# Optimization experiments

Measured on AMD Instinct MI355X. Metric: run time of the kernel, lower is better.

## Reference

```python
import jax, jax.numpy as jnp
import numpy as np
from jax import lax

B, S, H, T = 64, 512, 1024, 48


def setup_inputs() -> dict:
    key = jax.random.key(0)
    ks = jax.random.split(key, 8)
    x = jax.random.normal(ks[0], (B, S, H), dtype=jnp.float32)
    # left-aligned variable-length attention mask (lengths in [S//2, S])
    lengths = jax.random.randint(ks[1], (B,), S // 2, S + 1)
    attention_mask = (jnp.arange(S)[None, :] < lengths[:, None]).astype(jnp.int32)
    labels = jax.random.randint(ks[2], (B, S), 0, T).astype(jnp.int64)
    # decoder Linear(H, T)
    W = jax.random.normal(ks[3], (H, T), dtype=jnp.float32) / np.sqrt(H)
    b = jnp.zeros((T,), dtype=jnp.float32)
    # CRF parameters (allennlp-style: transitions + start/end transitions)
    transitions = jax.random.normal(ks[4], (T, T), dtype=jnp.float32) * 0.1
    start_trans = jax.random.normal(ks[5], (T,), dtype=jnp.float32) * 0.1
    end_trans = jax.random.normal(ks[6], (T,), dtype=jnp.float32) * 0.1
    return {"x": x, "attention_mask": attention_mask, "labels": labels,
            "W": W, "b": b, "transitions": transitions,
            "start_trans": start_trans, "end_trans": end_trans}


def _log_partition(logits, mask, trans, start, end):
    # logits [B,S,T], mask [B,S] int. Returns logZ [B].
    alpha0 = start[None, :] + logits[:, 0]                     # [B,T]
    emits = jnp.moveaxis(logits[:, 1:], 1, 0)                  # [S-1,B,T]
    ms = mask[:, 1:].T                                         # [S-1,B]

    def step(alpha, inp):
        emit, m = inp
        inner = alpha[:, :, None] + trans[None, :, :] + emit[:, None, :]  # [B,T,T]
        new = jax.nn.logsumexp(inner, axis=1)
        alpha = jnp.where(m[:, None] > 0, new, alpha)
        return alpha, None

    alpha, _ = lax.scan(step, alpha0, (emits, ms))
    return jax.nn.logsumexp(alpha + end[None, :], axis=1)      # [B]


def _gold_score(logits, labels, mask, trans, start, end):
    maskf = mask.astype(logits.dtype)
    emit = jnp.take_along_axis(logits, labels[..., None], axis=2)[..., 0]  # [B,S]
    emit_score = jnp.sum(emit * maskf, axis=1)
    tr = trans[labels[:, :-1], labels[:, 1:]]                   # [B,S-1]
    trans_score = jnp.sum(tr * maskf[:, 1:], axis=1)
    last_idx = jnp.sum(mask, axis=1) - 1                        # [B]
    last_tags = jnp.take_along_axis(labels, last_idx[:, None], axis=1)[:, 0]
    return start[labels[:, 0]] + emit_score + trans_score + end[last_tags]


def _viterbi(logits, mask, trans, start, end):
    Bn, Sn, Tn = logits.shape
    v0 = start[None, :] + logits[:, 0]
    emits = jnp.moveaxis(logits[:, 1:], 1, 0)                  # [S-1,B,T]
    ms = mask[:, 1:].T
    ident = jnp.broadcast_to(jnp.arange(Tn, dtype=jnp.int32)[None, :], (Bn, Tn))

    def step(v, inp):
        emit, m = inp
        scores = v[:, :, None] + trans[None, :, :]              # [B,T_prev,T_cur]
        bp = jnp.argmax(scores, axis=1).astype(jnp.int32)       # [B,T]
        best = jnp.max(scores, axis=1) + emit
        v_new = jnp.where(m[:, None] > 0, best, v)
        bp = jnp.where(m[:, None] > 0, bp, ident)               # identity at padded steps
        return v_new, bp

    v, bps = lax.scan(step, v0, (emits, ms))                    # bps [S-1,B,T]
    last = jnp.argmax(v + end[None, :], axis=1).astype(jnp.int32)  # [B]

    def back(tag, bp):
        prev = jnp.take_along_axis(bp, tag[:, None], axis=1)[:, 0]
        return prev, tag

    first_tag, rest = lax.scan(back, last, bps, reverse=True)   # rest [S-1,B]
    tags = jnp.concatenate([first_tag[:, None], rest.T], axis=1)  # [B,S]
    return (tags * mask).astype(jnp.int64)                      # pad with zeros


def reference(x, attention_mask, labels, W, b, transitions, start_trans, end_trans):
    features = jnp.einsum('bsh,ht->bst', x, W) + b              # decoder Linear
    pred_labels = _viterbi(features, attention_mask, transitions, start_trans, end_trans)
    logZ = _log_partition(features, attention_mask, transitions, start_trans, end_trans)
    gold = _gold_score(features, labels, attention_mask, transitions, start_trans, end_trans)
    loss = -jnp.sum(gold - logZ)                                # -log-likelihood, summed over batch
    return features, pred_labels, loss
```

## Files before the change

### kernel.cpp

```cpp
#include <hip/hip_runtime.h>
#include <hip/hip_bf16.h>
#include <math.h>

#define Bn 64
#define Sn 512
#define Hn 1024
#define Tn 48

#define LOG2E 1.4426950408889634f
#define LN2f  0.6931471805599453f

#define PRED_OFF (Bn*Sn*Tn)
#define LOSS_OFF (PRED_OFF + Bn*Sn)

#define RL(x,i) __int_as_float(__builtin_amdgcn_readlane(__float_as_int(x),(i)))

#if __has_builtin(__builtin_amdgcn_exp2f)
#define EXP2(x) __builtin_amdgcn_exp2f(x)
#else
#define EXP2(x) exp2f(x)
#endif
#if __has_builtin(__builtin_amdgcn_logf)
#define LOG2(x) __builtin_amdgcn_logf(x)
#else
#define LOG2(x) log2f(x)
#endif

#define DOT4(ACC,A,B) { ACC = fmaf((A).x,(B).x,ACC); ACC = fmaf((A).y,(B).y,ACC); ACC = fmaf((A).z,(B).z,ACC); ACC = fmaf((A).w,(B).w,ACC); }

__global__ __launch_bounds__(256) void gemm_feat(
    const float* __restrict__ x, const float* __restrict__ W,
    const float* __restrict__ bias, float* __restrict__ feat)
{
  __shared__ __align__(16) float xs[64][68];
  __shared__ __align__(16) float wsT[Tn][68];
  const int tid = threadIdx.x;
  const int srow = tid >> 2;
  const int sqc  = tid & 3;
  const int ty = tid >> 3;
  const int tx = tid & 7;
  const size_t row0 = (size_t)blockIdx.x * 64;

  float4 xreg[4];
  float  wreg[12];
  #pragma unroll
  for (int p = 0; p < 4; ++p)
    xreg[p] = *reinterpret_cast<const float4*>(&x[(row0 + srow)*Hn + (sqc + p*4)*4]);
  #pragma unroll
  for (int i = 0; i < 12; ++i) {
    const int id = tid + i*256; const int kk = id/Tn; const int t = id - kk*Tn;
    wreg[i] = W[(size_t)kk*Tn + t];
  }

  float acc[2][6];
  #pragma unroll
  for (int r = 0; r < 2; ++r)
    #pragma unroll
    for (int c = 0; c < 6; ++c) acc[r][c] = 0.f;

  for (int k0 = 0; k0 < Hn; k0 += 64) {
    #pragma unroll
    for (int p = 0; p < 4; ++p)
      *reinterpret_cast<float4*>(&xs[srow][(sqc + p*4)*4]) = xreg[p];
    #pragma unroll
    for (int i = 0; i < 12; ++i) {
      const int id = tid + i*256; const int kk = id/Tn; const int t = id - kk*Tn;
      wsT[t][kk] = wreg[i];
    }
    __syncthreads();
    if (k0 + 64 < Hn) {
      #pragma unroll
      for (int p = 0; p < 4; ++p)
        xreg[p] = *reinterpret_cast<const float4*>(&x[(row0 + srow)*Hn + (k0+64) + (sqc + p*4)*4]);
      #pragma unroll
      for (int i = 0; i < 12; ++i) {
        const int id = tid + i*256; const int kk = id/Tn; const int t = id - kk*Tn;
        wreg[i] = W[(size_t)(k0 + 64 + kk)*Tn + t];
      }
    }
    #pragma unroll 4
    for (int kk = 0; kk < 64; kk += 4) {
      const float4 a0 = *reinterpret_cast<const float4*>(&xs[ty*2+0][kk]);
      const float4 a1 = *reinterpret_cast<const float4*>(&xs[ty*2+1][kk]);
      const float4 w0 = *reinterpret_cast<const float4*>(&wsT[tx*6+0][kk]);
      const float4 w1 = *reinterpret_cast<const float4*>(&wsT[tx*6+1][kk]);
      const float4 w2 = *reinterpret_cast<const float4*>(&wsT[tx*6+2][kk]);
      const float4 w3 = *reinterpret_cast<const float4*>(&wsT[tx*6+3][kk]);
      const float4 w4 = *reinterpret_cast<const float4*>(&wsT[tx*6+4][kk]);
      const float4 w5 = *reinterpret_cast<const float4*>(&wsT[tx*6+5][kk]);
      DOT4(acc[0][0],a0,w0) DOT4(acc[0][1],a0,w1) DOT4(acc[0][2],a0,w2)
      DOT4(acc[0][3],a0,w3) DOT4(acc[0][4],a0,w4) DOT4(acc[0][5],a0,w5)
      DOT4(acc[1][0],a1,w0) DOT4(acc[1][1],a1,w1) DOT4(acc[1][2],a1,w2)
      DOT4(acc[1][3],a1,w3) DOT4(acc[1][4],a1,w4) DOT4(acc[1][5],a1,w5)
    }
    __syncthreads();
  }
  #pragma unroll
  for (int c = 0; c < 6; ++c) {
    const int col = tx*6 + c;
    const float bv = bias[col];
    #pragma unroll
    for (int r = 0; r < 2; ++r)
      feat[(row0 + ty*2 + r)*Tn + col] = acc[r][c] + bv;
  }
}

__global__ __launch_bounds__(64, 1) void crf_kernel(
    const float* __restrict__ feat,
    const int* __restrict__ mask,
    const int* __restrict__ labels,
    const float* __restrict__ trans,
    const float* __restrict__ startv,
    const float* __restrict__ endv,
    float* __restrict__ pred_out,
    float* __restrict__ wsLogZ,
    float* __restrict__ wsGold)
{
  __shared__ unsigned char bpL[Sn * 64];
  __shared__ unsigned char pathL[384 * 64];
  __shared__ int EA[8];

  const int role = blockIdx.x >> 6;
  const int b    = blockIdx.x & 63;
  const int lane = threadIdx.x;
  const float* fb = feat + (size_t)b * Sn * Tn;

  int lc = 0;
  #pragma unroll
  for (int it = 0; it < Sn/64; ++it) lc += (mask[(size_t)b*Sn + it*64 + lane] != 0);
  #pragma unroll
  for (int off = 32; off; off >>= 1) lc += __shfl_xor(lc, off);
  const int len = lc;

  const int j = (lane < Tn) ? lane : (Tn - 1);

  if (role == 0) {
    float Ev[48];
    #pragma unroll
    for (int i = 0; i < 48; ++i) Ev[i] = EXP2(trans[i*Tn + j] * LOG2E);
    const float a0 = (startv[j] + fb[j]) * LOG2E;
    float Zref = RL(a0, 0);
    float beta = a0 - Zref;
    float em2 = fb[Tn + j] * LOG2E;
    for (int t = 1; t < len; ++t) {
      const int tn = (t + 1 < len) ? (t + 1) : t;
      const float em_nxt = fb[(size_t)tn*Tn + j] * LOG2E;
      const float p = EXP2(beta);
      float s0=0.f, s1=0.f, s2=0.f, s3=0.f;
      #pragma unroll
      for (int i = 0; i < 48; i += 4) {
        s0 = fmaf(RL(p, i+0), Ev[i+0], s0);
        s1 = fmaf(RL(p, i+1), Ev[i+1], s1);
        s2 = fmaf(RL(p, i+2), Ev[i+2], s2);
        s3 = fmaf(RL(p, i+3), Ev[i+3], s3);
      }
      const float dj = LOG2((s0 + s1) + (s2 + s3)) + em2;
      const float d0 = RL(dj, 0);
      Zref += d0;
      beta = dj - d0;
      em2 = em_nxt;
    }
    float fv = (lane < Tn) ? beta + endv[lane] * LOG2E : -INFINITY;
    float m = fv;
    #pragma unroll
    for (int off = 32; off; off >>= 1) m = fmaxf(m, __shfl_xor(m, off));
    float e = (lane < Tn) ? EXP2(fv - m) : 0.f;
    #pragma unroll
    for (int off = 32; off; off >>= 1) e += __shfl_xor(e, off);
    if (lane == 0) wsLogZ[b] = (Zref + m + LOG2(e)) * LN2f;

  } else if (role == 1) {
    float trv[48];
    #pragma unroll
    for (int i = 0; i < 48; ++i) trv[i] = trans[i*Tn + j];
    float v = startv[j] + fb[j];
    float em_cur = fb[Tn + j];
    for (int t = 1; t < len; ++t) {
      const int tn = (t + 1 < len) ? (t + 1) : t;
      const float em_nxt = fb[(size_t)tn*Tn + j];
      float bestA = -INFINITY, bestB = -INFINITY;
      int idxA = 0, idxB = 0;
      #pragma unroll
      for (int k = 0; k < 12; ++k) {
        const float q0 = RL(v, 4*k+0) + trv[4*k+0];
        const float q1 = RL(v, 4*k+1) + trv[4*k+1];
        const float q2 = RL(v, 4*k+2) + trv[4*k+2];
        const float q3 = RL(v, 4*k+3) + trv[4*k+3];
        float gv = q0; int gi = 4*k;
        bool g1 = q1 > gv; gv = g1 ? q1 : gv; gi = g1 ? 4*k+1 : gi;
        bool g2 = q2 > gv; gv = g2 ? q2 : gv; gi = g2 ? 4*k+2 : gi;
        bool g3 = q3 > gv; gv = g3 ? q3 : gv; gi = g3 ? 4*k+3 : gi;
        if ((k & 1) == 0) { bool g = gv > bestA; bestA = g ? gv : bestA; idxA = g ? gi : idxA; }
        else              { bool g = gv > bestB; bestB = g ? gv : bestB; idxB = g ? gi : idxB; }
      }
      float best; int bidx;
      if (bestB > bestA || (bestB == bestA && idxB < idxA)) { best = bestB; bidx = idxB; }
      else                                                  { best = bestA; bidx = idxA; }
      bpL[t*64 + lane] = (unsigned char)bidx;
      v = best + em_cur;
      em_cur = em_nxt;
    }
    for (int t = len; t < Sn; ++t) bpL[t*64 + lane] = (unsigned char)lane;

    float fv = (lane < Tn) ? v + endv[lane] : -INFINITY;
    int fi = (lane < Tn) ? lane : 64;
    #pragma unroll
    for (int off = 32; off; off >>= 1) {
      const float ov = __shfl_xor(fv, off);
      const int   oi = __shfl_xor(fi, off);
      if (ov > fv || (ov == fv && oi < fi)) { fv = ov; fi = oi; }
    }
    __syncthreads();

    #define JOB(r) \
      const int id##r  = lane + 64*(r); \
      const int seg##r = id##r & 7;     \
      int cur##r = id##r >> 3;          \
      const int bpb##r = seg##r << 12;  \
      const int pb##r  = id##r << 6;    \
      pathL[pb##r + 63] = (unsigned char)cur##r;
    JOB(0) JOB(1) JOB(2) JOB(3) JOB(4) JOB(5)
    for (int d = 62; d >= 0; --d) {
      const int o = (d + 1) << 6;
      cur0 = bpL[bpb0 + o + cur0]; pathL[pb0 + d] = (unsigned char)cur0;
      cur1 = bpL[bpb1 + o + cur1]; pathL[pb1 + d] = (unsigned char)cur1;
      cur2 = bpL[bpb2 + o + cur2]; pathL[pb2 + d] = (unsigned char)cur2;
      cur3 = bpL[bpb3 + o + cur3]; pathL[pb3 + d] = (unsigned char)cur3;
      cur4 = bpL[bpb4 + o + cur4]; pathL[pb4 + d] = (unsigned char)cur4;
      cur5 = bpL[bpb5 + o + cur5]; pathL[pb5 + d] = (unsigned char)cur5;
    }
    #undef JOB
    __syncthreads();
    if (lane == 0) {
      int Ecur = fi;
      EA[7] = Ecur;
      for (int s = 7; s >= 1; --s) {
        const int bottom = pathL[((Ecur << 3) + s) * 64];
        Ecur = bpL[(s << 12) + bottom];
        EA[s-1] = Ecur;
      }
    }
    __syncthreads();
    #pragma unroll
    for (int r8 = 0; r8 < 8; ++r8) {
      const int t = r8*64 + lane;
      const int pv = pathL[((EA[r8] << 3) + r8) * 64 + lane];
      pred_out[(size_t)b*Sn + t] = (t < len) ? (float)pv : 0.f;
    }

  } else {
    float g = 0.f;
    #pragma unroll
    for (int it = 0; it < Sn/64; ++it) {
      const int sg = it*64 + lane;
      if (sg < len) {
        const int la = labels[(size_t)b*Sn + sg];
        float e = fb[(size_t)sg*Tn + la];
        if (sg > 0) e += trans[labels[(size_t)b*Sn + sg - 1]*Tn + la];
        g += e;
      }
    }
    #pragma unroll
    for (int off = 32; off; off >>= 1) g += __shfl_xor(g, off);
    if (lane == 0) {
      g += startv[labels[(size_t)b*Sn]] + endv[labels[(size_t)b*Sn + len - 1]];
      wsGold[b] = g;
    }
  }
}

__global__ void loss_reduce(const float* __restrict__ wsLogZ,
                            const float* __restrict__ wsGold,
                            float* __restrict__ out)
{
  const int lane = threadIdx.x;
  float v = wsLogZ[lane] - wsGold[lane];
  #pragma unroll
  for (int off = 32; off; off >>= 1) v += __shfl_xor(v, off);
  if (lane == 0) out[0] = v;
}

extern "C" void kernel_launch(void* const* d_in, const int* in_sizes, int n_in,
                              void* d_out, int out_size, void* d_ws, size_t ws_size,
                              hipStream_t stream) {
  const float* x      = (const float*)d_in[0];
  const int*   mask   = (const int*)  d_in[1];
  const int*   labels = (const int*)  d_in[2];
  const float* W      = (const float*)d_in[3];
  const float* bias   = (const float*)d_in[4];
  const float* trans  = (const float*)d_in[5];
  const float* startv = (const float*)d_in[6];
  const float* endv   = (const float*)d_in[7];

  float* out  = (float*)d_out;
  float* feat = out;
  float* pred = out + PRED_OFF;
  float* loss = out + LOSS_OFF;
  float* wsLogZ = (float*)d_ws;
  float* wsGold = wsLogZ + 64;

  gemm_feat<<<(Bn*Sn)/64, 256, 0, stream>>>(x, W, bias, feat);
  crf_kernel<<<192, 64, 0, stream>>>(feat, mask, labels, trans, startv, endv, pred, wsLogZ, wsGold);
  loss_reduce<<<1, 64, 0, stream>>>(wsLogZ, wsGold, loss);
}
```

Measured before the change: 356.1 us.

## Enlarge GEMM register tile and make Viterbi argmax branch-free with max3 trees

The feature GEMM now runs 128 threads per block, each computing a 4x6 output tile instead of 2x6. The x tile is stored transposed as float4 columns with padding, which cuts LDS traffic per FMA and adds reuse. The Viterbi inner step now takes a flat max over all 48 candidates via a max3-friendly tree, then finds the first index equal to the max with a min tree, replacing the sequential compare-select chain. The tie-breaking order is kept, but register pressure grows and GEMM occupancy may drop.

Result: no change. 349.9 us (-1.8%).

```diff
diff --git a/kernel.cpp b/kernel.cpp
--- a/kernel.cpp
+++ b/kernel.cpp
@@ -26,72 +26,81 @@
 #define LOG2(x) log2f(x)
 #endif
 
-#define DOT4(ACC,A,B) { ACC = fmaf((A).x,(B).x,ACC); ACC = fmaf((A).y,(B).y,ACC); ACC = fmaf((A).z,(B).z,ACC); ACC = fmaf((A).w,(B).w,ACC); }
-
-__global__ __launch_bounds__(256) void gemm_feat(
+__device__ __forceinline__ int imin(int a, int b) { return a < b ? a : b; }
+
+__global__ __launch_bounds__(128) void gemm_feat(
     const float* __restrict__ x, const float* __restrict__ W,
     const float* __restrict__ bias, float* __restrict__ feat)
 {
-  __shared__ __align__(16) float xs[64][68];
+  __shared__ __align__(16) float4 xs2[16][80];
   __shared__ __align__(16) float wsT[Tn][68];
   const int tid = threadIdx.x;
-  const int srow = tid >> 2;
-  const int sqc  = tid & 3;
+  const int tx = tid & 7;
   const int ty = tid >> 3;
-  const int tx = tid & 7;
   const size_t row0 = (size_t)blockIdx.x * 64;
-
-  float4 xreg[4];
-  float  wreg[12];
-  #pragma unroll
-  for (int p = 0; p < 4; ++p)
-    xreg[p] = *reinterpret_cast<const float4*>(&x[(row0 + srow)*Hn + (sqc + p*4)*4]);
-  #pragma unroll
-  for (int i = 0; i < 12; ++i) {
-    const int id = tid + i*256; const int kk = id/Tn; const int t = id - kk*Tn;
+  const int srow  = tid >> 1;
+  const int shalf = tid & 1;
+  const int srowp = srow + (srow >> 2);
+
+  float4 xreg[8];
+  float  wreg[24];
+  #pragma unroll
+  for (int p = 0; p < 8; ++p)
+    xreg[p] = *reinterpret_cast<const float4*>(&x[(row0 + srow)*Hn + (shalf*8 + p)*4]);
+  #pragma unroll
+  for (int i = 0; i < 24; ++i) {
+    const int id = tid + i*128; const int kk = id/Tn; const int t = id - kk*Tn;
     wreg[i] = W[(size_t)kk*Tn + t];
   }
 
-  float acc[2][6];
-  #pragma unroll
-  for (int r = 0; r < 2; ++r)
+  float acc[4][6];
+  #pragma unroll
+  for (int r = 0; r < 4; ++r)
     #pragma unroll
     for (int c = 0; c < 6; ++c) acc[r][c] = 0.f;
 
   for (int k0 = 0; k0 < Hn; k0 += 64) {
     #pragma unroll
-    for (int p = 0; p < 4; ++p)
-      *reinterpret_cast<float4*>(&xs[srow][(sqc + p*4)*4]) = xreg[p];
-    #pragma unroll
-    for (int i = 0; i < 12; ++i) {
-      const int id = tid + i*256; const int kk = id/Tn; const int t = id - kk*Tn;
+    for (int p = 0; p < 8; ++p)
+      xs2[shalf*8 + p][srowp] = xreg[p];
+    #pragma unroll
+    for (int i = 0; i < 24; ++i) {
+      const int id = tid + i*128; const int kk = id/Tn; const int t = id - kk*Tn;
       wsT[t][kk] = wreg[i];
     }
     __syncthreads();
     if (k0 + 64 < Hn) {
       #pragma unroll
-      for (int p = 0; p < 4; ++p)
-        xreg[p] = *reinterpret_cast<const float4*>(&x[(row0 + srow)*Hn + (k0+64) + (sqc + p*4)*4]);
-      #pragma unroll
-      for (int i = 0; i < 12; ++i) {
-        const int id = tid + i*256; const int kk = id/Tn; const int t = id - kk*Tn;
+      for (int p = 0; p < 8; ++p)
+        xreg[p] = *reinterpret_cast<const float4*>(&x[(row0 + srow)*Hn + (k0+64) + (shalf*8 + p)*4]);
+      #pragma unroll
+      for (int i = 0; i < 24; ++i) {
+        const int id = tid + i*128; const int kk = id/Tn; const int t = id - kk*Tn;
         wreg[i] = W[(size_t)(k0 + 64 + kk)*Tn + t];
       }
     }
-    #pragma unroll 4
-    for (int kk = 0; kk < 64; kk += 4) {
-      const float4 a0 = *reinterpret_cast<const float4*>(&xs[ty*2+0][kk]);
-      const float4 a1 = *reinterpret_cast<const float4*>(&xs[ty*2+1][kk]);
-      const float4 w0 = *reinterpret_cast<const float4*>(&wsT[tx*6+0][kk]);
-      const float4 w1 = *reinterpret_cast<const float4*>(&wsT[tx*6+1][kk]);
-      const float4 w2 = *reinterpret_cast<const float4*>(&wsT[tx*6+2][kk]);
-      const float4 w3 = *reinterpret_cast<const float4*>(&wsT[tx*6+3][kk]);
-      const float4 w4 = *reinterpret_cast<const float4*>(&wsT[tx*6+4][kk]);
-      const float4 w5 = *reinterpret_cast<const float4*>(&wsT[tx*6+5][kk]);
-      DOT4(acc[0][0],a0,w0) DOT4(acc[0][1],a0,w1) DOT4(acc[0][2],a0,w2)
-      DOT4(acc[0][3],a0,w3) DOT4(acc[0][4],a0,w4) DOT4(acc[0][5],a0,w5)
-      DOT4(acc[1][0],a1,w0) DOT4(acc[1][1],a1,w1) DOT4(acc[1][2],a1,w2)
-      DOT4(acc[1][3],a1,w3) DOT4(acc[1][4],a1,w4) DOT4(acc[1][5],a1,w5)
+    #pragma unroll
+    for (int kk4 = 0; kk4 < 16; ++kk4) {
+      const float4 a0 = xs2[kk4][5*ty + 0];
+      const float4 a1 = xs2[kk4][5*ty + 1];
+      const float4 a2 = xs2[kk4][5*ty + 2];
+      const float4 a3 = xs2[kk4][5*ty + 3];
+      const float4 w0 = *reinterpret_cast<const float4*>(&wsT[tx*6+0][kk4*4]);
+      const float4 w1 = *reinterpret_cast<const float4*>(&wsT[tx*6+1][kk4*4]);
+      const float4 w2 = *reinterpret_cast<const float4*>(&wsT[tx*6+2][kk4*4]);
+      const float4 w3 = *reinterpret_cast<const float4*>(&wsT[tx*6+3][kk4*4]);
+      const float4 w4 = *reinterpret_cast<const float4*>(&wsT[tx*6+4][kk4*4]);
+      const float4 w5 = *reinterpret_cast<const float4*>(&wsT[tx*6+5][kk4*4]);
+      #define FMA4(ACC,A,B) { ACC = fmaf((A).x,(B).x,ACC); ACC = fmaf((A).y,(B).y,ACC); ACC = fmaf((A).z,(B).z,ACC); ACC = fmaf((A).w,(B).w,ACC); }
+      FMA4(acc[0][0],a0,w0) FMA4(acc[0][1],a0,w1) FMA4(acc[0][2],a0,w2)
+      FMA4(acc[0][3],a0,w3) FMA4(acc[0][4],a0,w4) FMA4(acc[0][5],a0,w5)
+      FMA4(acc[1][0],a1,w0) FMA4(acc[1][1],a1,w1) FMA4(acc[1][2],a1,w2)
+      FMA4(acc[1][3],a1,w3) FMA4(acc[1][4],a1,w4) FMA4(acc[1][5],a1,w5)
+      FMA4(acc[2][0],a2,w0) FMA4(acc[2][1],a2,w1) FMA4(acc[2][2],a2,w2)
+      FMA4(acc[2][3],a2,w3) FMA4(acc[2][4],a2,w4) FMA4(acc[2][5],a2,w5)
+      FMA4(acc[3][0],a3,w0) FMA4(acc[3][1],a3,w1) FMA4(acc[3][2],a3,w2)
+      FMA4(acc[3][3],a3,w3) FMA4(acc[3][4],a3,w4) FMA4(acc[3][5],a3,w5)
+      #undef FMA4
     }
     __syncthreads();
   }
@@ -100,8 +109,8 @@
     const int col = tx*6 + c;
     const float bv = bias[col];
     #pragma unroll
-    for (int r = 0; r < 2; ++r)
-      feat[(row0 + ty*2 + r)*Tn + col] = acc[r][c] + bv;
+    for (int r = 0; r < 4; ++r)
+      feat[(row0 + ty*4 + r)*Tn + col] = acc[r][c] + bv;
   }
 }
 
@@ -178,24 +187,36 @@
     for (int t = 1; t < len; ++t) {
       const int tn = (t + 1 < len) ? (t + 1) : t;
       const float em_nxt = fb[(size_t)tn*Tn + j];
-      float bestA = -INFINITY, bestB = -INFINITY;
-      int idxA = 0, idxB = 0;
-      #pragma unroll
-      for (int k = 0; k < 12; ++k) {
-        const float q0 = RL(v, 4*k+0) + trv[4*k+0];
-        const float q1 = RL(v, 4*k+1) + trv[4*k+1];
-        const float q2 = RL(v, 4*k+2) + trv[4*k+2];
-        const float q3 = RL(v, 4*k+3) + trv[4*k+3];
-        float gv = q0; int gi = 4*k;
-        bool g1 = q1 > gv; gv = g1 ? q1 : gv; gi = g1 ? 4*k+1 : gi;
-        bool g2 = q2 > gv; gv = g2 ? q2 : gv; gi = g2 ? 4*k+2 : gi;
-        bool g3 = q3 > gv; gv = g3 ? q3 : gv; gi = g3 ? 4*k+3 : gi;
-        if ((k & 1) == 0) { bool g = gv > bestA; bestA = g ? gv : bestA; idxA = g ? gi : idxA; }
-        else              { bool g = gv > bestB; bestB = g ? gv : bestB; idxB = g ? gi : idxB; }
-      }
-      float best; int bidx;
-      if (bestB > bestA || (bestB == bestA && idxB < idxA)) { best = bestB; bidx = idxB; }
-      else                                                  { best = bestA; bidx = idxA; }
+      float q[48];
+      #pragma unroll
+      for (int i = 0; i < 48; ++i) q[i] = RL(v, i) + trv[i];
+      float m16[16];
+      #pragma unroll
+      for (int u = 0; u < 16; ++u)
+        m16[u] = fmaxf(fmaxf(q[3*u], q[3*u+1]), q[3*u+2]);
+      float m6a = fmaxf(fmaxf(m16[0],  m16[1]),  m16[2]);
+      float m6b = fmaxf(fmaxf(m16[3],  m16[4]),  m16[5]);
+      float m6c = fmaxf(fmaxf(m16[6],  m16[7]),  m16[8]);
+      float m6d = fmaxf(fmaxf(m16[9],  m16[10]), m16[11]);
+      float m6e = fmaxf(fmaxf(m16[12], m16[13]), m16[14]);
+      float m6f = m16[15];
+      const float best = fmaxf(fmaxf(fmaxf(m6a,m6b),m6c),
+                               fmaxf(fmaxf(m6d,m6e),m6f));
+      int s16[16];
+      #pragma unroll
+      for (int u = 0; u < 16; ++u) {
+        int a = (q[3*u]   == best) ? (3*u)   : 63;
+        int bq = (q[3*u+1] == best) ? (3*u+1) : 63;
+        int cq = (q[3*u+2] == best) ? (3*u+2) : 63;
+        s16[u] = imin(imin(a, bq), cq);
+      }
+      int i6a = imin(imin(s16[0],  s16[1]),  s16[2]);
+      int i6b = imin(imin(s16[3],  s16[4]),  s16[5]);
+      int i6c = imin(imin(s16[6],  s16[7]),  s16[8]);
+      int i6d = imin(imin(s16[9],  s16[10]), s16[11]);
+      int i6e = imin(imin(s16[12], s16[13]), s16[14]);
+      int i6f = s16[15];
+      const int bidx = imin(imin(imin(i6a,i6b),i6c), imin(imin(i6d,i6e),i6f));
       bpL[t*64 + lane] = (unsigned char)bidx;
       v = best + em_cur;
       em_cur = em_nxt;
@@ -299,7 +320,7 @@
   float* wsLogZ = (float*)d_ws;
   float* wsGold = wsLogZ + 64;
 
-  gemm_feat<<<(Bn*Sn)/64, 256, 0, stream>>>(x, W, bias, feat);
+  gemm_feat<<<(Bn*Sn)/64, 128, 0, stream>>>(x, W, bias, feat);
   crf_kernel<<<192, 64, 0, stream>>>(feat, mask, labels, trans, startv, endv, pred, wsLogZ, wsGold);
   loss_reduce<<<1, 64, 0, stream>>>(wsLogZ, wsGold, loss);
 }
```
